# Optimization experiments

Hardware: AMD Instinct MI355X
Metric: run time of the kernel (lower is better)

The kernel has to match this reference:

```python
import jax, jax.numpy as jnp
import numpy as np

NUM_HEADS = 16
NUM_KV_HEADS = 4
HEAD_DIM = 128
TOP_K = 4
RMS_EPS = 1e-6
ROPE_THETA = 10000.0


def setup_inputs() -> dict:
    key = jax.random.key(0)
    ks = jax.random.split(key, 10)
    T, h, E, I, SI = 1024, 2048, 16, 512, 1024
    s = 0.02  # weight init scale for numerical sanity
    return {
        "hidden_states": jax.random.normal(ks[0], (T, h), jnp.float32),
        "residual": jax.random.normal(ks[1], (T, h), jnp.float32),
        "rms1_w": jnp.ones((h,), jnp.float32),
        "rms2_w": jnp.ones((h,), jnp.float32),
        "w_qkv": jax.random.normal(ks[2], (h, NUM_HEADS * HEAD_DIM + 2 * NUM_KV_HEADS * HEAD_DIM), jnp.float32) * s,
        "w_dense": jax.random.normal(ks[3], (NUM_HEADS * HEAD_DIM, h), jnp.float32) * s,
        "gate_w": jax.random.normal(ks[4], (h, E), jnp.float32) * s,
        "w13": jax.random.normal(ks[5], (E, h, 2 * I), jnp.float32) * s,
        "w2": jax.random.normal(ks[6], (E, I, h), jnp.float32) * s,
        "sw13": jax.random.normal(ks[7], (h, 2 * SI), jnp.float32) * s,
        "sw2": jax.random.normal(ks[8], (SI, h), jnp.float32) * s,
        "position_ids": jnp.arange(T, dtype=jnp.int32),
    }


def _rmsnorm(x, w, eps=RMS_EPS):
    var = jnp.mean(jnp.square(x), axis=-1, keepdims=True)
    return x * jax.lax.rsqrt(var + eps) * w


def _rope_neox(pos, x):
    # x: [T, H, D]; rotate-half (neox) style over full head_dim
    d = x.shape[-1]
    inv_freq = 1.0 / (ROPE_THETA ** (jnp.arange(0, d, 2, dtype=jnp.float32) / d))  # [d/2]
    ang = pos.astype(jnp.float32)[:, None] * inv_freq  # [T, d/2]
    cos = jnp.cos(ang)[:, None, :]  # [T, 1, d/2]
    sin = jnp.sin(ang)[:, None, :]
    x1, x2 = x[..., : d // 2], x[..., d // 2 :]
    return jnp.concatenate([x1 * cos - x2 * sin, x2 * cos + x1 * sin], axis=-1)


def reference(hidden_states, residual, rms1_w, rms2_w, w_qkv, w_dense,
              gate_w, w13, w2, sw13, sw2, position_ids):
    T, h = hidden_states.shape
    q_size = NUM_HEADS * HEAD_DIM
    kv_size = NUM_KV_HEADS * HEAD_DIM

    # --- input RMSNorm with fused residual add ---
    resid = hidden_states + residual
    x = _rmsnorm(resid, rms1_w)

    # --- attention ---
    qkv = x @ w_qkv
    q = qkv[:, :q_size].reshape(T, NUM_HEADS, HEAD_DIM)
    k = qkv[:, q_size : q_size + kv_size].reshape(T, NUM_KV_HEADS, HEAD_DIM)
    v = qkv[:, q_size + kv_size :].reshape(T, NUM_KV_HEADS, HEAD_DIM)
    q = _rope_neox(position_ids, q)
    k = _rope_neox(position_ids, k)
    rep = NUM_HEADS // NUM_KV_HEADS
    kr = jnp.repeat(k, rep, axis=1)  # [T, H, D]
    vr = jnp.repeat(v, rep, axis=1)
    scale = HEAD_DIM ** -0.5
    scores = jnp.einsum('thd,shd->hts', q, kr) * scale  # [H, T, T]
    causal = jnp.tril(jnp.ones((T, T), dtype=bool))
    scores = jnp.where(causal[None], scores, -1e9)
    probs = jax.nn.softmax(scores, axis=-1)
    ctx = jnp.einsum('hts,shd->thd', probs, vr).reshape(T, q_size)
    attn_out = ctx @ w_dense

    # --- post-attention RMSNorm with fused residual add ---
    resid2 = attn_out + resid
    x2 = _rmsnorm(resid2, rms2_w)

    # --- shared experts (SiLU-and-mul MLP) ---
    gu = x2 @ sw13
    sg, su = jnp.split(gu, 2, axis=-1)
    shared = (jax.nn.silu(sg) * su) @ sw2

    # --- MoE routing: softmax -> top-k -> renormalize ---
    E = gate_w.shape[1]
    router_probs = jax.nn.softmax(x2 @ gate_w, axis=-1)  # [T, E]
    topk_w, topk_ids = jax.lax.top_k(router_probs, TOP_K)
    topk_w = topk_w / jnp.sum(topk_w, axis=-1, keepdims=True)
    comb = jnp.zeros((T, E), x2.dtype).at[jnp.arange(T)[:, None], topk_ids].add(topk_w)

    # --- experts (dense grouped-GEMM equivalent, combined by routing weights) ---
    h_all = jnp.einsum('td,edf->etf', x2, w13)  # [E, T, 2I]
    eg, eu = jnp.split(h_all, 2, axis=-1)
    act = jax.nn.silu(eg) * eu  # [E, T, I]
    moe = jnp.einsum('etf,efh,te->th', act, w2, comb)

    return (moe + shared, resid2)
```

## Files before the change

kernel.cpp:

```cpp
#include <hip/hip_runtime.h>
#include <math.h>

#define HD 2048
#define NQH 16
#define NKVH 4
#define HEADD 128
#define QKVN 3072
#define NEXP 16
#define EI 512
#define SSI 1024
#define TOPK 4
#define TT 1024

typedef __bf16 bf16x8 __attribute__((ext_vector_type(8)));
typedef float f32x4 __attribute__((ext_vector_type(4)));
typedef unsigned short u16x8 __attribute__((ext_vector_type(8)));

static __device__ __forceinline__ unsigned short f2bf(float f) {
    union { float f; unsigned int u; } v; v.f = f;
    unsigned int r = v.u + 0x7fff + ((v.u >> 16) & 1);
    return (unsigned short)(r >> 16);
}

static __device__ __forceinline__ void gl_lds16(const unsigned short* g,
                                                unsigned short* l) {
    __builtin_amdgcn_global_load_lds(
        (const __attribute__((address_space(1))) unsigned int*)g,
        (__attribute__((address_space(3))) unsigned int*)l, 16, 0, 0);
}

__global__ __launch_bounds__(256) void add_rmsnorm_kernel(
    const float* __restrict__ a, const float* __restrict__ b,
    const float* __restrict__ w, float* __restrict__ resid_out,
    unsigned short* __restrict__ x_bf)
{
    int t = blockIdx.x;
    int tid = threadIdx.x;
    const float4* a4 = (const float4*)(a + (size_t)t * HD);
    const float4* b4 = b ? (const float4*)(b + (size_t)t * HD) : nullptr;
    float4* r4 = resid_out ? (float4*)(resid_out + (size_t)t * HD) : nullptr;
    const float4* w4 = (const float4*)w;

    float4 v[2];
    float ss = 0.f;
#pragma unroll
    for (int l = 0; l < 2; ++l) {
        int idx = tid + l * 256;
        float4 va = a4[idx];
        if (b4) {
            float4 vb = b4[idx];
            va.x += vb.x; va.y += vb.y; va.z += vb.z; va.w += vb.w;
        }
        if (r4) r4[idx] = va;
        v[l] = va;
        ss += va.x * va.x + va.y * va.y + va.z * va.z + va.w * va.w;
    }
    for (int off = 32; off > 0; off >>= 1) ss += __shfl_down(ss, off);
    __shared__ float red[4];
    int lane = tid & 63, wv = tid >> 6;
    if (lane == 0) red[wv] = ss;
    __syncthreads();
    if (tid == 0) {
        float s = red[0] + red[1] + red[2] + red[3];
        red[0] = rsqrtf(s / (float)HD + 1e-6f);
    }
    __syncthreads();
    float inv = red[0];
#pragma unroll
    for (int l = 0; l < 2; ++l) {
        int idx = tid + l * 256;
        float4 va = v[l], vw = w4[idx];
        ushort4 ob;
        ob.x = f2bf(va.x * inv * vw.x);
        ob.y = f2bf(va.y * inv * vw.y);
        ob.z = f2bf(va.z * inv * vw.z);
        ob.w = f2bf(va.w * inv * vw.w);
        ((ushort4*)(x_bf + (size_t)t * HD))[idx] = ob;
    }
}

__global__ __launch_bounds__(256) void reduce4_add_rmsnorm(
    const float* __restrict__ part, const float* __restrict__ resid,
    const float* __restrict__ w, float* __restrict__ resid2_out,
    unsigned short* __restrict__ x_bf)
{
    const size_t NP = (size_t)TT * HD / 4;
    int t = blockIdx.x;
    int tid = threadIdx.x;
    const float4* p4 = (const float4*)part;
    const float4* r4 = (const float4*)(resid + (size_t)t * HD);
    float4* o4 = (float4*)(resid2_out + (size_t)t * HD);
    const float4* w4 = (const float4*)w;

    float4 v[2];
    float ss = 0.f;
#pragma unroll
    for (int l = 0; l < 2; ++l) {
        int li = tid + l * 256;
        size_t idx = (size_t)t * (HD / 4) + li;
        float4 s = p4[idx];
        float4 q1 = p4[NP + idx], q2 = p4[2 * NP + idx], q3 = p4[3 * NP + idx];
        float4 rr = r4[li];
        s.x += q1.x + q2.x + q3.x + rr.x;
        s.y += q1.y + q2.y + q3.y + rr.y;
        s.z += q1.z + q2.z + q3.z + rr.z;
        s.w += q1.w + q2.w + q3.w + rr.w;
        o4[li] = s;
        v[l] = s;
        ss += s.x * s.x + s.y * s.y + s.z * s.z + s.w * s.w;
    }
    for (int off = 32; off > 0; off >>= 1) ss += __shfl_down(ss, off);
    __shared__ float red[4];
    int lane = tid & 63, wv = tid >> 6;
    if (lane == 0) red[wv] = ss;
    __syncthreads();
    if (tid == 0) {
        float s = red[0] + red[1] + red[2] + red[3];
        red[0] = rsqrtf(s / (float)HD + 1e-6f);
    }
    __syncthreads();
    float inv = red[0];
#pragma unroll
    for (int l = 0; l < 2; ++l) {
        int li = tid + l * 256;
        float4 va = v[l], vw = w4[li];
        ushort4 ob;
        ob.x = f2bf(va.x * inv * vw.x);
        ob.y = f2bf(va.y * inv * vw.y);
        ob.z = f2bf(va.z * inv * vw.z);
        ob.w = f2bf(va.w * inv * vw.w);
        ((ushort4*)(x_bf + (size_t)t * HD))[li] = ob;
    }
}

__global__ __launch_bounds__(256) void transpose_convert(
    const float* __restrict__ in, unsigned short* __restrict__ out,
    int K, int N, long long strideIn, long long strideOut)
{
    __shared__ float tile[64][33];
    const int n0 = blockIdx.x * 32;
    const int k0 = blockIdx.y * 64;
    const float* ip = in + (size_t)blockIdx.z * strideIn;
    unsigned short* op = out + (size_t)blockIdx.z * strideOut;
    int tid = threadIdx.x;
    int c = (tid & 7) * 4;
#pragma unroll
    for (int i = 0; i < 2; ++i) {
        int r = (tid >> 3) + i * 32;
        float4 v = *(const float4*)(ip + (size_t)(k0 + r) * N + n0 + c);
        tile[r][c] = v.x; tile[r][c + 1] = v.y;
        tile[r][c + 2] = v.z; tile[r][c + 3] = v.w;
    }
    __syncthreads();
    int rr = tid >> 3;
    int kc = (tid & 7) * 8;
    u16x8 o;
#pragma unroll
    for (int j = 0; j < 8; ++j) o[j] = f2bf(tile[kc + j][rr]);
    *(u16x8*)(op + (size_t)(n0 + rr) * K + k0 + kc) = o;
}

#define SBK 64

__global__ __launch_bounds__(256) void gemm_splitk(
    const unsigned short* __restrict__ A, const unsigned short* __restrict__ B,
    float* __restrict__ Cpart, int M, int N, int Kc, int ldA, int ldB)
{
    __shared__ unsigned short As[2][128 * SBK];
    __shared__ unsigned short Bs[2][128 * SBK];

    const int tid = threadIdx.x;
    const int wave = tid >> 6;
    const int lane = tid & 63;
    const int wr = wave >> 1, wc = wave & 1;
    const int l15 = lane & 15;
    const int row0 = blockIdx.y * 128;
    const int col0 = blockIdx.x * 128;
    const int z = blockIdx.z;

    const unsigned short* Ap = A + (size_t)row0 * ldA + (size_t)z * Kc;
    const unsigned short* Bp = B + (size_t)col0 * ldB + (size_t)z * Kc;

    const int r_st = tid >> 3;
    const int q_st = tid & 7;
    const int csrc = (q_st ^ (r_st & 7)) << 3;

    f32x4 acc[4][4] = {};

    const int nsteps = Kc / SBK;

#define STAGE_SK(buf, k0s)                                                    \
    {                                                                         \
        _Pragma("unroll")                                                     \
        for (int i = 0; i < 4; ++i) {                                         \
            int rr = r_st + i * 32;                                           \
            gl_lds16(Ap + (size_t)rr * ldA + (k0s) + csrc,                    \
                     &As[buf][rr * SBK + q_st * 8]);                          \
            gl_lds16(Bp + (size_t)rr * ldB + (k0s) + csrc,                    \
                     &Bs[buf][rr * SBK + q_st * 8]);                          \
        }                                                                     \
    }

    STAGE_SK(0, 0);

    for (int s = 0; s < nsteps; ++s) {
        const int cur = s & 1;
        if (s + 1 < nsteps) {
            STAGE_SK(cur ^ 1, (s + 1) * SBK);
            asm volatile("s_waitcnt vmcnt(8)" ::: "memory");
        } else {
            asm volatile("s_waitcnt vmcnt(0)" ::: "memory");
        }
        __builtin_amdgcn_s_barrier();

#pragma unroll
        for (int half = 0; half < 2; ++half) {
            const int q = half * 4 + (lane >> 4);
            bf16x8 af[4], bfv[4];
#pragma unroll
            for (int i = 0; i < 4; ++i) {
                int R = wr * 64 + i * 16 + l15;
                af[i] = *(const bf16x8*)&As[cur][R * SBK + ((q ^ (R & 7)) << 3)];
            }
#pragma unroll
            for (int j = 0; j < 4; ++j) {
                int R = wc * 64 + j * 16 + l15;
                bfv[j] = *(const bf16x8*)&Bs[cur][R * SBK + ((q ^ (R & 7)) << 3)];
            }
#pragma unroll
            for (int mi = 0; mi < 4; ++mi)
#pragma unroll
                for (int nj = 0; nj < 4; ++nj)
                    acc[mi][nj] = __builtin_amdgcn_mfma_f32_16x16x32_bf16(
                        af[mi], bfv[nj], acc[mi][nj], 0, 0, 0);
        }
        __builtin_amdgcn_s_barrier();
    }

    float* Cp = Cpart + (size_t)z * M * N;
#pragma unroll
    for (int mi = 0; mi < 4; ++mi)
#pragma unroll
        for (int nj = 0; nj < 4; ++nj)
#pragma unroll
            for (int r = 0; r < 4; ++r) {
                int row = row0 + wr * 64 + mi * 16 + (lane >> 4) * 4 + r;
                int col = col0 + wc * 64 + nj * 16 + l15;
                Cp[(size_t)row * N + col] = acc[mi][nj][r];
            }
}

__global__ __launch_bounds__(256) void reduce_partials(
    const float* __restrict__ part, int ns, int n4,
    const float* __restrict__ add, float* __restrict__ out, int acc)
{
    const float4* p4 = (const float4*)part;
    const float4* a4 = (const float4*)add;
    float4* o4 = (float4*)out;
    for (int idx = blockIdx.x * 256 + threadIdx.x; idx < n4;
         idx += gridDim.x * 256) {
        float4 s = p4[idx];
        for (int z = 1; z < ns; ++z) {
            float4 q = p4[(size_t)z * n4 + idx];
            s.x += q.x; s.y += q.y; s.z += q.z; s.w += q.w;
        }
        if (add) {
            float4 q = a4[idx];
            s.x += q.x; s.y += q.y; s.z += q.z; s.w += q.w;
        }
        if (acc) {
            float4 q = o4[idx];
            s.x += q.x; s.y += q.y; s.z += q.z; s.w += q.w;
        }
        o4[idx] = s;
    }
}

__global__ __launch_bounds__(256) void reduce_swiglu(
    const float* __restrict__ part, int ns, unsigned short* __restrict__ out)
{
    int idx4 = blockIdx.x * 256 + threadIdx.x;
    int t = idx4 >> 8;
    int i4 = (idx4 & 255) * 4;
    const float4* pg = (const float4*)(part + (size_t)t * (2 * SSI) + i4);
    const float4* pu = (const float4*)(part + (size_t)t * (2 * SSI) + SSI + i4);
    float4 g = pg[0], u = pu[0];
    for (int z = 1; z < ns; ++z) {
        float4 g2 = *(const float4*)((const float*)pg + (size_t)z * TT * 2 * SSI);
        float4 u2 = *(const float4*)((const float*)pu + (size_t)z * TT * 2 * SSI);
        g.x += g2.x; g.y += g2.y; g.z += g2.z; g.w += g2.w;
        u.x += u2.x; u.y += u2.y; u.z += u2.z; u.w += u2.w;
    }
    ushort4 o;
    o.x = f2bf((g.x / (1.f + __expf(-g.x))) * u.x);
    o.y = f2bf((g.y / (1.f + __expf(-g.y))) * u.y);
    o.z = f2bf((g.z / (1.f + __expf(-g.z))) * u.z);
    o.w = f2bf((g.w / (1.f + __expf(-g.w))) * u.w);
    *(ushort4*)(out + (size_t)t * SSI + i4) = o;
}

__global__ __launch_bounds__(256) void build_lists(
    const float* __restrict__ comb, int* __restrict__ lists,
    int* __restrict__ slots, int* __restrict__ cnts)
{
    int e = blockIdx.x;
    int tid = threadIdx.x;
    __shared__ int sc[256];
    int loc[4];
    int c = 0;
#pragma unroll
    for (int j = 0; j < 4; ++j) {
        int t = tid * 4 + j;
        if (comb[(size_t)t * NEXP + e] > 0.f) loc[c++] = t;
    }
    sc[tid] = c;
    __syncthreads();
    for (int off = 1; off < 256; off <<= 1) {
        int v = (tid >= off) ? sc[tid - off] : 0;
        __syncthreads();
        sc[tid] += v;
        __syncthreads();
    }
    int base = sc[tid] - c;
    for (int i = 0; i < c; ++i) {
        int t = loc[i];
        int s = 0;
        for (int e2 = 0; e2 < e; ++e2)
            s += (comb[(size_t)t * NEXP + e2] > 0.f) ? 1 : 0;
        lists[e * TT + base + i] = t;
        slots[e * TT + base + i] = s;
    }
    if (tid == 255) cnts[e] = sc[255];
}

__global__ void scan_cnts(const int* __restrict__ cnts, int* __restrict__ bases)
{
    if (threadIdx.x == 0 && blockIdx.x == 0) {
        int a = 0;
        for (int e = 0; e < NEXP; ++e) { bases[e] = a; a += cnts[e]; }
        bases[NEXP] = a;
    }
}

__global__ __launch_bounds__(256) void moe_up_gather(
    const unsigned short* __restrict__ x2B,
    const unsigned short* __restrict__ w13T,
    const float* __restrict__ comb,
    const int* __restrict__ lists,
    const int* __restrict__ cnts,
    const int* __restrict__ bases,
    unsigned short* __restrict__ actC)
{
    __shared__ unsigned short As[2][64 * 64];
    __shared__ unsigned short Bgs[2][64 * 64];
    __shared__ unsigned short Bus[2][64 * 64];

    const int e = blockIdx.z;
    const int cnt = cnts[e];
    const int m0 = blockIdx.y * 64;
    if (m0 >= cnt) return;
    const int n0 = blockIdx.x * 64;
    const int base_e = bases[e];

    const int tid = threadIdx.x;
    const int w = tid >> 6;
    const int lane = tid & 63;
    const int l15 = lane & 15;
    const int g = lane >> 4;

    const int r0 = tid >> 3;
    const int q_st = tid & 7;
    const int swz = (q_st ^ (r0 & 7)) << 3;

    int a0 = m0 + r0, a1 = m0 + r0 + 32;
    int tok0 = lists[e * TT + (a0 < cnt ? a0 : cnt - 1)];
    int tok1 = lists[e * TT + (a1 < cnt ? a1 : cnt - 1)];
    const unsigned short* Asrc0 = x2B + (size_t)tok0 * HD;
    const unsigned short* Asrc1 = x2B + (size_t)tok1 * HD;
    const unsigned short* Bbase = w13T + (size_t)e * 1024 * HD;
    const unsigned short* Bg0 = Bbase + (size_t)(n0 + r0) * HD;
    const unsigned short* Bg1 = Bbase + (size_t)(n0 + r0 + 32) * HD;
    const unsigned short* Bu0 = Bg0 + (size_t)512 * HD;
    const unsigned short* Bu1 = Bg1 + (size_t)512 * HD;

    f32x4 ag[4] = {};
    f32x4 au[4] = {};

#define STAGE_UP(buf, k0s)                                                    \
    {                                                                         \
        gl_lds16(Asrc0 + (k0s) + swz, &As[buf][(tid) * 8]);                   \
        gl_lds16(Asrc1 + (k0s) + swz, &As[buf][(tid + 256) * 8]);             \
        gl_lds16(Bg0 + (k0s) + swz, &Bgs[buf][(tid) * 8]);                    \
        gl_lds16(Bg1 + (k0s) + swz, &Bgs[buf][(tid + 256) * 8]);              \
        gl_lds16(Bu0 + (k0s) + swz, &Bus[buf][(tid) * 8]);                    \
        gl_lds16(Bu1 + (k0s) + swz, &Bus[buf][(tid + 256) * 8]);              \
    }

    STAGE_UP(0, 0);

    const int nsteps = HD / 64;
    for (int s = 0; s < nsteps; ++s) {
        const int cur = s & 1;
        if (s + 1 < nsteps) {
            STAGE_UP(cur ^ 1, (s + 1) * 64);
            asm volatile("s_waitcnt vmcnt(6)" ::: "memory");
        } else {
            asm volatile("s_waitcnt vmcnt(0)" ::: "memory");
        }
        __builtin_amdgcn_s_barrier();

#pragma unroll
        for (int kk2 = 0; kk2 < 2; ++kk2) {
            const int q = kk2 * 4 + g;
            bf16x8 af[4], bg, bu;
#pragma unroll
            for (int i = 0; i < 4; ++i) {
                int R = i * 16 + l15;
                af[i] = *(const bf16x8*)&As[cur][R * 64 + ((q ^ (R & 7)) << 3)];
            }
            {
                int R = w * 16 + l15;
                int off = R * 64 + ((q ^ (R & 7)) << 3);
                bg = *(const bf16x8*)&Bgs[cur][off];
                bu = *(const bf16x8*)&Bus[cur][off];
            }
#pragma unroll
            for (int mi = 0; mi < 4; ++mi) {
                ag[mi] = __builtin_amdgcn_mfma_f32_16x16x32_bf16(
                    af[mi], bg, ag[mi], 0, 0, 0);
                au[mi] = __builtin_amdgcn_mfma_f32_16x16x32_bf16(
                    af[mi], bu, au[mi], 0, 0, 0);
            }
        }
        __builtin_amdgcn_s_barrier();
    }

#pragma unroll
    for (int mi = 0; mi < 4; ++mi) {
#pragma unroll
        for (int r = 0; r < 4; ++r) {
            int grow = m0 + mi * 16 + g * 4 + r;
            if (grow >= cnt) continue;
            int tok = lists[e * TT + grow];
            float cw = comb[(size_t)tok * NEXP + e];
            int col = n0 + w * 16 + l15;
            float gg = ag[mi][r];
            float uu = au[mi][r];
            float v = (gg / (1.f + __expf(-gg))) * uu * cw;
            actC[(size_t)(base_e + grow) * EI + col] = f2bf(v);
        }
    }
}

__global__ __launch_bounds__(256) void moe_down_gather(
    const unsigned short* __restrict__ actC,
    const unsigned short* __restrict__ w2T,
    const int* __restrict__ lists,
    const int* __restrict__ slots,
    const int* __restrict__ cnts,
    const int* __restrict__ bases,
    float* __restrict__ slotpart)
{
    __shared__ unsigned short As[2][64 * 64];
    __shared__ unsigned short Bs[2][128 * 64];

    const int e = blockIdx.z;
    const int cnt = cnts[e];
    const int m0 = blockIdx.y * 64;
    if (m0 >= cnt) return;
    const int n0 = blockIdx.x * 128;
    const int base_e = bases[e];

    const int tid = threadIdx.x;
    const int w = tid >> 6;
    const int lane = tid & 63;
    const int l15 = lane & 15;
    const int g = lane >> 4;

    const int r0 = tid >> 3;
    const int q_st = tid & 7;
    const int swz = (q_st ^ (r0 & 7)) << 3;

    int a0 = m0 + r0, a1 = m0 + r0 + 32;
    const unsigned short* Asrc0 =
        actC + (size_t)(base_e + (a0 < cnt ? a0 : cnt - 1)) * EI;
    const unsigned short* Asrc1 =
        actC + (size_t)(base_e + (a1 < cnt ? a1 : cnt - 1)) * EI;
    const unsigned short* Bbase = w2T + (size_t)e * EI;

#define STAGE_DN(buf, k0s)                                                    \
    {                                                                         \
        gl_lds16(Asrc0 + (k0s) + swz, &As[buf][(tid) * 8]);                   \
        gl_lds16(Asrc1 + (k0s) + swz, &As[buf][(tid + 256) * 8]);             \
        _Pragma("unroll")                                                     \
        for (int i = 0; i < 4; ++i) {                                         \
            int rr = r0 + i * 32;                                             \
            gl_lds16(Bbase + (size_t)(n0 + rr) * (NEXP * EI) + (k0s) + swz,   \
                     &Bs[buf][(tid + i * 256) * 8]);                          \
        }                                                                     \
    }

    f32x4 acc[4][2] = {};

    STAGE_DN(0, 0);

    const int nsteps = EI / 64;
    for (int s = 0; s < nsteps; ++s) {
        const int cur = s & 1;
        if (s + 1 < nsteps) {
            STAGE_DN(cur ^ 1, (s + 1) * 64);
            asm volatile("s_waitcnt vmcnt(6)" ::: "memory");
        } else {
            asm volatile("s_waitcnt vmcnt(0)" ::: "memory");
        }
        __builtin_amdgcn_s_barrier();

#pragma unroll
        for (int kk2 = 0; kk2 < 2; ++kk2) {
            const int q = kk2 * 4 + g;
            bf16x8 af[4], bf[2];
#pragma unroll
            for (int i = 0; i < 4; ++i) {
                int R = i * 16 + l15;
                af[i] = *(const bf16x8*)&As[cur][R * 64 + ((q ^ (R & 7)) << 3)];
            }
#pragma unroll
            for (int j = 0; j < 2; ++j) {
                int R = w * 32 + j * 16 + l15;
                bf[j] = *(const bf16x8*)&Bs[cur][R * 64 + ((q ^ (R & 7)) << 3)];
            }
#pragma unroll
            for (int mi = 0; mi < 4; ++mi)
#pragma unroll
                for (int nj = 0; nj < 2; ++nj)
                    acc[mi][nj] = __builtin_amdgcn_mfma_f32_16x16x32_bf16(
                        af[mi], bf[nj], acc[mi][nj], 0, 0, 0);
        }
        __builtin_amdgcn_s_barrier();
    }

#pragma unroll
    for (int mi = 0; mi < 4; ++mi) {
#pragma unroll
        for (int r = 0; r < 4; ++r) {
            int grow = m0 + mi * 16 + g * 4 + r;
            if (grow >= cnt) continue;
            int tok = lists[e * TT + grow];
            int sl  = slots[e * TT + grow];
            float* orow = slotpart + (size_t)sl * TT * HD + (size_t)tok * HD;
#pragma unroll
            for (int nj = 0; nj < 2; ++nj) {
                int col = n0 + w * 32 + nj * 16 + l15;
                orow[col] = acc[mi][nj][r];
            }
        }
    }
}

__global__ __launch_bounds__(256) void rope_pack(
    const float* __restrict__ qkv0, const float* __restrict__ qkv1,
    const int* __restrict__ pos_ids,
    unsigned short* __restrict__ Qb, unsigned short* __restrict__ Kb,
    unsigned short* __restrict__ Vb)
{
    const float SCALE = 0.08838834764831843f;
    int t = blockIdx.x;
    int tid = threadIdx.x;
    int w = tid >> 6, lane = tid & 63;
    float pos = (float)pos_ids[t];
    float invf = powf(10000.0f, -(float)lane * (1.0f / 64.0f));
    float ang = pos * invf;
    float c = cosf(ang);
    float s = sinf(ang);
    const float* row0 = qkv0 + (size_t)t * QKVN;
    const float* row1 = qkv1 + (size_t)t * QKVN;
#pragma unroll
    for (int j = 0; j < 5; ++j) {
        int hh = w * 5 + j;
        const float* hb0 = row0 + hh * HEADD;
        const float* hb1 = row1 + hh * HEADD;
        float x1 = hb0[lane] + hb1[lane];
        float x2 = hb0[lane + 64] + hb1[lane + 64];
        float o1 = x1 * c - x2 * s;
        float o2 = x2 * c + x1 * s;
        if (hh < NQH) {
            unsigned short* qp = Qb + ((size_t)hh * TT + t) * HEADD;
            qp[lane] = f2bf(o1 * SCALE);
            qp[lane + 64] = f2bf(o2 * SCALE);
        } else {
            unsigned short* kp = Kb + ((size_t)(hh - NQH) * TT + t) * HEADD;
            kp[lane] = f2bf(o1);
            kp[lane + 64] = f2bf(o2);
        }
    }
    float2 v0 = *(const float2*)(row0 + 2560 + tid * 2);
    float2 v1 = *(const float2*)(row1 + 2560 + tid * 2);
    int kvh = tid >> 6;
    int d = (tid * 2) & 127;
    unsigned int packed = (unsigned int)f2bf(v0.x + v1.x) |
                          ((unsigned int)f2bf(v0.y + v1.y) << 16);
    *(unsigned int*)(Vb + ((size_t)kvh * TT + t) * HEADD + d) = packed;
}

__global__ __launch_bounds__(256) void transpose_v(
    const unsigned short* __restrict__ Vb, unsigned short* __restrict__ Vt)
{
    __shared__ unsigned short tile[32][40];
    const int kvh = blockIdx.z;
    const int t0 = blockIdx.x * 32, d0 = blockIdx.y * 32;
    int tid = threadIdx.x;
    int r = tid >> 3, c4 = (tid & 7) * 4;
    ushort4 v = *(const ushort4*)(Vb + ((size_t)kvh * TT + t0 + r) * HEADD + d0 + c4);
    tile[r][c4] = v.x; tile[r][c4 + 1] = v.y;
    tile[r][c4 + 2] = v.z; tile[r][c4 + 3] = v.w;
    __syncthreads();
    ushort4 o;
    o.x = tile[c4 + 0][r];
    o.y = tile[c4 + 1][r];
    o.z = tile[c4 + 2][r];
    o.w = tile[c4 + 3][r];
    *(ushort4*)(Vt + ((size_t)kvh * HEADD + d0 + r) * TT + t0 + c4) = o;
}

__global__ __launch_bounds__(128) void flash_attn_mfma(
    const unsigned short* __restrict__ Qb,
    const unsigned short* __restrict__ Kb,
    const unsigned short* __restrict__ Vt,
    unsigned short* __restrict__ ctx)
{
    __shared__ __align__(16) unsigned short Ks[2][64 * 128];
    __shared__ __align__(16) unsigned short Vs[2][128 * 64];
    __shared__ __align__(16) unsigned short Pl[2][16][72];

    const int h   = blockIdx.x;
    const int p   = blockIdx.y;
    const int rh  = blockIdx.z;
    const int kvh = h >> 2;
    const int tid = threadIdx.x;
    const int w   = tid >> 6;
    const int lane = tid & 63;
    const int l15 = lane & 15;
    const int g   = lane >> 4;

    const unsigned short* Kh = Kb + (size_t)kvh * TT * HEADD;
    const unsigned short* Vh = Vt + (size_t)kvh * HEADD * TT;

#define STAGE_KV(buf, s0s)                                                    \
    {                                                                         \
        _Pragma("unroll")                                                     \
        for (int i = 0; i < 8; ++i) {                                         \
            int idx = tid + i * 128;                                          \
            int r = idx >> 4, c = idx & 15;                                   \
            int csw = (c & 8) | ((c ^ r) & 7);                                \
            gl_lds16(Kh + (size_t)((s0s) + r) * HEADD + csw * 8,              \
                     &Ks[buf][idx * 8]);                                      \
        }                                                                     \
        _Pragma("unroll")                                                     \
        for (int i = 0; i < 8; ++i) {                                         \
            int idx = tid + i * 128;                                          \
            int r = idx >> 3, c = idx & 7;                                    \
            int csw = (c ^ r) & 7;                                            \
            gl_lds16(Vh + (size_t)r * TT + (s0s) + csw * 8,                   \
                     &Vs[buf][idx * 8]);                                      \
        }                                                                     \
    }

    const int qts[2] = {p, 15 - p};

#pragma unroll
    for (int qi = 0; qi < 2; ++qi) {
        const int qt = qts[qi];
        const int q0 = qt * 64 + rh * 32 + w * 16;
        const int ntiles = qt + 1;

        const unsigned short* Qrow = Qb + ((size_t)h * TT + q0 + l15) * HEADD;
        bf16x8 qf[4];
#pragma unroll
        for (int kk = 0; kk < 4; ++kk)
            qf[kk] = *(const bf16x8*)(Qrow + kk * 32 + g * 8);

        float m_i[4], l_i[4];
#pragma unroll
        for (int r = 0; r < 4; ++r) { m_i[r] = -1e30f; l_i[r] = 0.f; }
        f32x4 of[8] = {};

        STAGE_KV(0, 0);

        for (int st = 0; st < ntiles; ++st) {
            const int cur = st & 1;
            const int s0 = st * 64;
            if (st + 1 < ntiles) {
                STAGE_KV(cur ^ 1, (st + 1) * 64);
                asm volatile("s_waitcnt vmcnt(16)" ::: "memory");
            } else {
                asm volatile("s_waitcnt vmcnt(0)" ::: "memory");
            }
            __builtin_amdgcn_s_barrier();

            f32x4 sacc[4] = {};
#pragma unroll
            for (int kk = 0; kk < 4; ++kk) {
#pragma unroll
                for (int n = 0; n < 4; ++n) {
                    int R = n * 16 + l15;
                    int cidx = kk * 4 + g;
                    int cs = (cidx & 8) | ((cidx ^ R) & 7);
                    bf16x8 kb = *(const bf16x8*)&Ks[cur][R * 128 + cs * 8];
                    sacc[n] = __builtin_amdgcn_mfma_f32_16x16x32_bf16(
                        qf[kk], kb, sacc[n], 0, 0, 0);
                }
            }

            const bool diag = (st == qt);
            float alpha[4];
#pragma unroll
            for (int r = 0; r < 4; ++r) {
                const int qrow = q0 + g * 4 + r;
                float sv[4] = {sacc[0][r], sacc[1][r], sacc[2][r], sacc[3][r]};
                if (diag) {
#pragma unroll
                    for (int n = 0; n < 4; ++n)
                        if (s0 + n * 16 + l15 > qrow) sv[n] = -1e30f;
                }
                float rm = fmaxf(fmaxf(sv[0], sv[1]), fmaxf(sv[2], sv[3]));
                rm = fmaxf(rm, __shfl_xor(rm, 1));
                rm = fmaxf(rm, __shfl_xor(rm, 2));
                rm = fmaxf(rm, __shfl_xor(rm, 4));
                rm = fmaxf(rm, __shfl_xor(rm, 8));
                float mnew = fmaxf(m_i[r], rm);
                alpha[r] = __expf(m_i[r] - mnew);
                float p0 = __expf(sv[0] - mnew);
                float p1 = __expf(sv[1] - mnew);
                float p2 = __expf(sv[2] - mnew);
                float p3 = __expf(sv[3] - mnew);
                float rs = p0 + p1 + p2 + p3;
                rs += __shfl_xor(rs, 1);
                rs += __shfl_xor(rs, 2);
                rs += __shfl_xor(rs, 4);
                rs += __shfl_xor(rs, 8);
                l_i[r] = l_i[r] * alpha[r] + rs;
                m_i[r] = mnew;
                Pl[w][g * 4 + r][0 * 16 + l15] = f2bf(p0);
                Pl[w][g * 4 + r][1 * 16 + l15] = f2bf(p1);
                Pl[w][g * 4 + r][2 * 16 + l15] = f2bf(p2);
                Pl[w][g * 4 + r][3 * 16 + l15] = f2bf(p3);
            }

#pragma unroll
            for (int nd = 0; nd < 8; ++nd)
#pragma unroll
                for (int r = 0; r < 4; ++r)
                    of[nd][r] *= alpha[r];

#pragma unroll
            for (int kk2 = 0; kk2 < 2; ++kk2) {
                bf16x8 pa = *(const bf16x8*)&Pl[w][l15][kk2 * 32 + g * 8];
#pragma unroll
                for (int nd = 0; nd < 8; ++nd) {
                    int R = nd * 16 + l15;
                    int cidx = kk2 * 4 + g;
                    int cs = (cidx ^ R) & 7;
                    bf16x8 vb = *(const bf16x8*)&Vs[cur][R * 64 + cs * 8];
                    of[nd] = __builtin_amdgcn_mfma_f32_16x16x32_bf16(
                        pa, vb, of[nd], 0, 0, 0);
                }
            }
            __builtin_amdgcn_s_barrier();
        }

        float invl[4];
#pragma unroll
        for (int r = 0; r < 4; ++r) invl[r] = 1.f / l_i[r];
#pragma unroll
        for (int nd = 0; nd < 8; ++nd)
#pragma unroll
            for (int r = 0; r < 4; ++r) {
                int trow = q0 + g * 4 + r;
                ctx[(size_t)trow * (NQH * HEADD) + h * HEADD + nd * 16 + l15] =
                    f2bf(of[nd][r] * invl[r]);
            }
    }
}

__global__ __launch_bounds__(256) void router_fused(
    const float* __restrict__ resid2, const float* __restrict__ w,
    const float* __restrict__ gate_w, float* __restrict__ comb)
{
    int t = blockIdx.x;
    int tid = threadIdx.x;
    int lane = tid & 63, wv = tid >> 6;

    const float4* r4 = (const float4*)(resid2 + (size_t)t * HD);
    float4 xa = r4[tid * 2], xb = r4[tid * 2 + 1];
    float ss = xa.x * xa.x + xa.y * xa.y + xa.z * xa.z + xa.w * xa.w +
               xb.x * xb.x + xb.y * xb.y + xb.z * xb.z + xb.w * xb.w;
    for (int off = 32; off > 0; off >>= 1) ss += __shfl_down(ss, off);
    __shared__ float red[4];
    if (lane == 0) red[wv] = ss;
    __syncthreads();
    float inv = rsqrtf((red[0] + red[1] + red[2] + red[3]) / (float)HD + 1e-6f);

    const float4* w4 = (const float4*)w;
    float4 wa = w4[tid * 2], wb = w4[tid * 2 + 1];
    float xs[8] = {xa.x * wa.x * inv, xa.y * wa.y * inv, xa.z * wa.z * inv,
                   xa.w * wa.w * inv, xb.x * wb.x * inv, xb.y * wb.y * inv,
                   xb.z * wb.z * inv, xb.w * wb.w * inv};

    float acc[16] = {};
    int kbase = tid * 8;
#pragma unroll
    for (int j = 0; j < 8; ++j) {
        float xv = xs[j];
        const float4* wrow = (const float4*)(gate_w + (size_t)(kbase + j) * NEXP);
        float4 w0 = wrow[0], w1 = wrow[1], w2 = wrow[2], w3 = wrow[3];
        acc[0] += xv * w0.x;  acc[1] += xv * w0.y;  acc[2] += xv * w0.z;  acc[3] += xv * w0.w;
        acc[4] += xv * w1.x;  acc[5] += xv * w1.y;  acc[6] += xv * w1.z;  acc[7] += xv * w1.w;
        acc[8] += xv * w2.x;  acc[9] += xv * w2.y;  acc[10] += xv * w2.z; acc[11] += xv * w2.w;
        acc[12] += xv * w3.x; acc[13] += xv * w3.y; acc[14] += xv * w3.z; acc[15] += xv * w3.w;
    }
    __shared__ float red2[4][16];
#pragma unroll
    for (int e = 0; e < 16; ++e) {
        float v = acc[e];
        v += __shfl_xor(v, 1);
        v += __shfl_xor(v, 2);
        v += __shfl_xor(v, 4);
        v += __shfl_xor(v, 8);
        v += __shfl_xor(v, 16);
        v += __shfl_xor(v, 32);
        if (lane == 0) red2[wv][e] = v;
    }
    __syncthreads();

    if (tid == 0) {
        float l[NEXP];
#pragma unroll
        for (int e = 0; e < NEXP; ++e)
            l[e] = red2[0][e] + red2[1][e] + red2[2][e] + red2[3][e];
        int sel[TOPK];
        float selv[TOPK];
        bool used[NEXP] = {};
#pragma unroll
        for (int r = 0; r < TOPK; ++r) {
            int best = -1;
            float bv = -1e30f;
            for (int e = 0; e < NEXP; ++e)
                if (!used[e] && l[e] > bv) { bv = l[e]; best = e; }
            used[best] = true;
            sel[r] = best;
            selv[r] = bv;
        }
        float mx = selv[0];
        float wsum = 0.f, wvv[TOPK];
#pragma unroll
        for (int r = 0; r < TOPK; ++r) { wvv[r] = __expf(selv[r] - mx); wsum += wvv[r]; }
        float out16[NEXP] = {};
#pragma unroll
        for (int r = 0; r < TOPK; ++r) out16[sel[r]] = wvv[r] / wsum;
#pragma unroll
        for (int e = 0; e < NEXP; ++e) comb[(size_t)t * NEXP + e] = out16[e];
    }
}

extern "C" void kernel_launch(void* const* d_in, const int* in_sizes, int n_in,
                              void* d_out, int out_size, void* d_ws, size_t ws_size,
                              hipStream_t stream)
{
    const float* hidden   = (const float*)d_in[0];
    const float* residual = (const float*)d_in[1];
    const float* rms1_w   = (const float*)d_in[2];
    const float* rms2_w   = (const float*)d_in[3];
    const float* w_qkv    = (const float*)d_in[4];
    const float* w_dense  = (const float*)d_in[5];
    const float* gate_w   = (const float*)d_in[6];
    const float* w13      = (const float*)d_in[7];
    const float* w2       = (const float*)d_in[8];
    const float* sw13     = (const float*)d_in[9];
    const float* sw2      = (const float*)d_in[10];
    const int*   pos_ids  = (const int*)d_in[11];

    const int T = TT;

    float* out0 = (float*)d_out;
    float* out1 = (float*)d_out + (size_t)T * HD;

    char* base = (char*)d_ws;
    float*          residF = (float*)(base);
    unsigned short* xB     = (unsigned short*)(base + 8388608);
    unsigned short* ctxB   = (unsigned short*)(base + 12582912);
    unsigned short* actC   = (unsigned short*)(base);
    unsigned short* x2B    = (unsigned short*)(base + 29360128);
    unsigned short* sactB  = (unsigned short*)(base + 33554432);
    float*          comb   = (float*)(base + 35651584);
    float*          part   = (float*)(base + 35717120);
    unsigned short* Wbuf   = (unsigned short*)(base + 69271552);
    int*            lists  = (int*)(base + 139526144);
    int*            cnts   = (int*)(base + 139591680);
    int*            slots  = (int*)(base + 139591936);
    int*            bases  = (int*)(base + 139657472);

    unsigned short* Qb = (unsigned short*)(base + 35717120 + 25165824);
    unsigned short* Kb = Qb + (size_t)NQH * TT * HEADD;
    unsigned short* Vb = Kb + (size_t)NKVH * TT * HEADD;
    unsigned short* Vt = Vb + (size_t)NKVH * TT * HEADD;

    dim3 blk(256);

    add_rmsnorm_kernel<<<dim3(T), blk, 0, stream>>>(
        hidden, residual, rms1_w, residF, xB);

    transpose_convert<<<dim3(QKVN / 32, HD / 64), blk, 0, stream>>>(
        w_qkv, Wbuf, HD, QKVN, 0, 0);
    gemm_splitk<<<dim3(QKVN / 128, T / 128, 2), blk, 0, stream>>>(
        xB, Wbuf, part, T, QKVN, 1024, HD, HD);

    rope_pack<<<dim3(T), blk, 0, stream>>>(
        part, part + (size_t)T * QKVN, pos_ids, Qb, Kb, Vb);
    transpose_v<<<dim3(T / 32, HEADD / 32, NKVH), blk, 0, stream>>>(Vb, Vt);

    flash_attn_mfma<<<dim3(NQH, 8, 2), dim3(128), 0, stream>>>(Qb, Kb, Vt, ctxB);

    transpose_convert<<<dim3(HD / 32, HD / 64), blk, 0, stream>>>(
        w_dense, Wbuf, HD, HD, 0, 0);
    gemm_splitk<<<dim3(HD / 128, T / 128, 4), blk, 0, stream>>>(
        ctxB, Wbuf, part, T, HD, 512, HD, HD);
    reduce4_add_rmsnorm<<<dim3(T), blk, 0, stream>>>(
        part, residF, rms2_w, out1, x2B);

    router_fused<<<dim3(T), blk, 0, stream>>>(out1, rms2_w, gate_w, comb);
    build_lists<<<dim3(NEXP), blk, 0, stream>>>(comb, lists, slots, cnts);
    scan_cnts<<<dim3(1), dim3(64), 0, stream>>>(cnts, bases);

    transpose_convert<<<dim3(2 * SSI / 32, HD / 64), blk, 0, stream>>>(
        sw13, Wbuf, HD, 2 * SSI, 0, 0);
    gemm_splitk<<<dim3(HD / 128, T / 128, 4), blk, 0, stream>>>(
        x2B, Wbuf, part, T, 2 * SSI, 512, HD, HD);

    reduce_swiglu<<<dim3(T * SSI / 4 / 256), blk, 0, stream>>>(part, 4, sactB);

    transpose_convert<<<dim3(HD / 32, SSI / 64), blk, 0, stream>>>(
        sw2, Wbuf, SSI, HD, 0, 0);
    gemm_splitk<<<dim3(HD / 128, T / 128, 4), blk, 0, stream>>>(
        sactB, Wbuf, part, T, HD, 256, SSI, SSI);
    reduce_partials<<<dim3(1024), blk, 0, stream>>>(
        part, 4, T * HD / 4, nullptr, out0, 0);

    transpose_convert<<<dim3(1024 / 32, HD / 64, NEXP), blk, 0, stream>>>(
        w13, Wbuf, HD, 1024, (long long)HD * 1024, (long long)1024 * HD);
    moe_up_gather<<<dim3(EI / 64, 16, NEXP), blk, 0, stream>>>(
        x2B, Wbuf, comb, lists, cnts, bases, actC);

    transpose_convert<<<dim3(HD / 32, (NEXP * EI) / 64), blk, 0, stream>>>(
        w2, Wbuf, NEXP * EI, HD, 0, 0);
    moe_down_gather<<<dim3(HD / 128, 16, NEXP), blk, 0, stream>>>(
        actC, Wbuf, lists, slots, cnts, bases, part);
    reduce_partials<<<dim3(1024), blk, 0, stream>>>(
        part, 4, T * HD / 4, nullptr, out0, 1);
}
```

Measured before the change: 350.1 us.

## Fuse w13 fp32-to-bf16 transpose into MoE up-projection GEMM B-tile loads

Removes the separate transpose_convert pass over the expert w13 weights. The up-projection kernel now reads fp32 weights straight from global memory into registers, converts them to bf16 and writes them transposed into swizzled LDS during the main loop. This drops one full write and re-read of a 64 MB weight buffer. In exchange, each block re-reads fp32 weights, twice the bytes of bf16, and the register-staged B path adds conversion ALU work and an extra vmcnt(0) wait per step.

```diff
diff --git a/kernel.cpp b/kernel.cpp
--- a/kernel.cpp
+++ b/kernel.cpp
@@ -15,6 +15,7 @@
 typedef __bf16 bf16x8 __attribute__((ext_vector_type(8)));
 typedef float f32x4 __attribute__((ext_vector_type(4)));
 typedef unsigned short u16x8 __attribute__((ext_vector_type(8)));
+typedef unsigned short u16x4 __attribute__((ext_vector_type(4)));
 
 static __device__ __forceinline__ unsigned short f2bf(float f) {
     union { float f; unsigned int u; } v; v.f = f;
@@ -342,9 +343,9 @@
     }
 }
 
-__global__ __launch_bounds__(256) void moe_up_gather(
+__global__ __launch_bounds__(256) void moe_up_f32(
     const unsigned short* __restrict__ x2B,
-    const unsigned short* __restrict__ w13T,
+    const float* __restrict__ w13,
     const float* __restrict__ comb,
     const int* __restrict__ lists,
     const int* __restrict__ cnts,
@@ -377,60 +378,96 @@
     int tok1 = lists[e * TT + (a1 < cnt ? a1 : cnt - 1)];
     const unsigned short* Asrc0 = x2B + (size_t)tok0 * HD;
     const unsigned short* Asrc1 = x2B + (size_t)tok1 * HD;
-    const unsigned short* Bbase = w13T + (size_t)e * 1024 * HD;
-    const unsigned short* Bg0 = Bbase + (size_t)(n0 + r0) * HD;
-    const unsigned short* Bg1 = Bbase + (size_t)(n0 + r0 + 32) * HD;
-    const unsigned short* Bu0 = Bg0 + (size_t)512 * HD;
-    const unsigned short* Bu1 = Bg1 + (size_t)512 * HD;
+
+    const int bkb = (tid >> 4) * 4;
+    const int bn4 = (tid & 15) * 4;
+    const float* Wg = w13 + (size_t)e * HD * 1024 + n0 + bn4;
+    const float* Wu = Wg + 512;
 
     f32x4 ag[4] = {};
     f32x4 au[4] = {};
 
-#define STAGE_UP(buf, k0s)                                                    \
+    float4 bg4[4], bu4[4];
+
+#define STAGE_A_UP(buf, k0s)                                                  \
     {                                                                         \
         gl_lds16(Asrc0 + (k0s) + swz, &As[buf][(tid) * 8]);                   \
         gl_lds16(Asrc1 + (k0s) + swz, &As[buf][(tid + 256) * 8]);             \
-        gl_lds16(Bg0 + (k0s) + swz, &Bgs[buf][(tid) * 8]);                    \
-        gl_lds16(Bg1 + (k0s) + swz, &Bgs[buf][(tid + 256) * 8]);              \
-        gl_lds16(Bu0 + (k0s) + swz, &Bus[buf][(tid) * 8]);                    \
-        gl_lds16(Bu1 + (k0s) + swz, &Bus[buf][(tid + 256) * 8]);              \
-    }
-
-    STAGE_UP(0, 0);
+    }
+
+#define LOADB_UP(k0s)                                                         \
+    {                                                                         \
+        _Pragma("unroll")                                                     \
+        for (int j = 0; j < 4; ++j) {                                         \
+            bg4[j] = *(const float4*)(Wg + (size_t)((k0s) + bkb + j) * 1024); \
+            bu4[j] = *(const float4*)(Wu + (size_t)((k0s) + bkb + j) * 1024); \
+        }                                                                     \
+    }
+
+#define CVTWRITE_UP(buf)                                                      \
+    {                                                                         \
+        _Pragma("unroll")                                                     \
+        for (int i = 0; i < 4; ++i) {                                         \
+            int nl = bn4 + i;                                                 \
+            int c8 = (tid >> 4) ^ (nl & 15);                                  \
+            u16x4 pg, pu;                                                     \
+            pg[0] = f2bf(((const float*)&bg4[0])[i]);                         \
+            pg[1] = f2bf(((const float*)&bg4[1])[i]);                         \
+            pg[2] = f2bf(((const float*)&bg4[2])[i]);                         \
+            pg[3] = f2bf(((const float*)&bg4[3])[i]);                         \
+            pu[0] = f2bf(((const float*)&bu4[0])[i]);                         \
+            pu[1] = f2bf(((const float*)&bu4[1])[i]);                         \
+            pu[2] = f2bf(((const float*)&bu4[2])[i]);                         \
+            pu[3] = f2bf(((const float*)&bu4[3])[i]);                         \
+            *(u16x4*)&Bgs[buf][(nl * 16 + c8) * 4] = pg;                      \
+            *(u16x4*)&Bus[buf][(nl * 16 + c8) * 4] = pu;                      \
+        }                                                                     \
+    }
 
     const int nsteps = HD / 64;
+
+    STAGE_A_UP(0, 0);
+    LOADB_UP(0);
+    asm volatile("s_waitcnt vmcnt(0)" ::: "memory");
+    CVTWRITE_UP(0);
+    asm volatile("s_waitcnt lgkmcnt(0)" ::: "memory");
+    __builtin_amdgcn_s_barrier();
+
     for (int s = 0; s < nsteps; ++s) {
         const int cur = s & 1;
         if (s + 1 < nsteps) {
-            STAGE_UP(cur ^ 1, (s + 1) * 64);
-            asm volatile("s_waitcnt vmcnt(6)" ::: "memory");
-        } else {
-            asm volatile("s_waitcnt vmcnt(0)" ::: "memory");
-        }
-        __builtin_amdgcn_s_barrier();
+            STAGE_A_UP(cur ^ 1, (s + 1) * 64);
+            LOADB_UP((s + 1) * 64);
+        }
 
 #pragma unroll
         for (int kk2 = 0; kk2 < 2; ++kk2) {
             const int q = kk2 * 4 + g;
-            bf16x8 af[4], bg, bu;
+            bf16x8 af[4];
 #pragma unroll
             for (int i = 0; i < 4; ++i) {
                 int R = i * 16 + l15;
                 af[i] = *(const bf16x8*)&As[cur][R * 64 + ((q ^ (R & 7)) << 3)];
             }
-            {
-                int R = w * 16 + l15;
-                int off = R * 64 + ((q ^ (R & 7)) << 3);
-                bg = *(const bf16x8*)&Bgs[cur][off];
-                bu = *(const bf16x8*)&Bus[cur][off];
-            }
+            const int Rb = w * 16 + l15;
+            union { u16x4 h[2]; bf16x8 v; } ubg, ubu;
+            ubg.h[0] = *(const u16x4*)&Bgs[cur][(Rb * 16 + ((2 * q) ^ l15)) * 4];
+            ubg.h[1] = *(const u16x4*)&Bgs[cur][(Rb * 16 + ((2 * q + 1) ^ l15)) * 4];
+            ubu.h[0] = *(const u16x4*)&Bus[cur][(Rb * 16 + ((2 * q) ^ l15)) * 4];
+            ubu.h[1] = *(const u16x4*)&Bus[cur][(Rb * 16 + ((2 * q + 1) ^ l15)) * 4];
 #pragma unroll
             for (int mi = 0; mi < 4; ++mi) {
                 ag[mi] = __builtin_amdgcn_mfma_f32_16x16x32_bf16(
-                    af[mi], bg, ag[mi], 0, 0, 0);
+                    af[mi], ubg.v, ag[mi], 0, 0, 0);
                 au[mi] = __builtin_amdgcn_mfma_f32_16x16x32_bf16(
-                    af[mi], bu, au[mi], 0, 0, 0);
-            }
+                    af[mi], ubu.v, au[mi], 0, 0, 0);
+            }
+        }
+
+        if (s + 1 < nsteps) {
+            asm volatile("s_waitcnt vmcnt(0)" ::: "memory");
+            CVTWRITE_UP(cur ^ 1);
+            asm volatile("s_waitcnt lgkmcnt(0)" ::: "memory");
         }
         __builtin_amdgcn_s_barrier();
     }
@@ -945,10 +982,8 @@
     reduce_partials<<<dim3(1024), blk, 0, stream>>>(
         part, 4, T * HD / 4, nullptr, out0, 0);
 
-    transpose_convert<<<dim3(1024 / 32, HD / 64, NEXP), blk, 0, stream>>>(
-        w13, Wbuf, HD, 1024, (long long)HD * 1024, (long long)1024 * HD);
-    moe_up_gather<<<dim3(EI / 64, 16, NEXP), blk, 0, stream>>>(
-        x2B, Wbuf, comb, lists, cnts, bases, actC);
+    moe_up_f32<<<dim3(EI / 64, 16, NEXP), blk, 0, stream>>>(
+        x2B, w13, comb, lists, cnts, bases, actC);
 
     transpose_convert<<<dim3(HD / 32, (NEXP * EI) / 64), blk, 0, stream>>>(
         w2, Wbuf, NEXP * EI, HD, 0, 0);
```

Measured after the change: 382.0 us. 9.1% more time.
